# Performance work log

Measured on AMD Instinct MI355X. Metric: run time of the kernel, lower is better.

## Reference

```python
import jax, jax.numpy as jnp
import numpy as np

DIM_U1 = 20
DIM_U2 = 20
DZ = 6
BATCH = 4096


def _mlp(x, Wa, ba, Wb, bb, Wc, bc, Wd, bd):
    h = jax.nn.relu(x @ Wa + ba)
    h = jax.nn.relu(h @ Wb + bb)
    h = jax.nn.relu(h @ Wc + bc)
    return h @ Wd + bd


def setup_inputs() -> dict:
    key = jax.random.key(0)
    ks = jax.random.split(key, 9)

    def lin(k, fan_in, fan_out):
        k1, k2 = jax.random.split(k)
        lim = 1.0 / np.sqrt(fan_in)
        W = jax.random.uniform(k1, (fan_in, fan_out), minval=-lim, maxval=lim, dtype=jnp.float32)
        b = jax.random.uniform(k2, (fan_out,), minval=-lim, maxval=lim, dtype=jnp.float32)
        return W, b

    d = {"x": jax.random.normal(ks[0], (BATCH, DIM_U1), dtype=jnp.float32)}
    dims1 = [(3, 16), (16, 32), (32, 16), (16, 1 + DZ * 3)]
    dims2 = [(3, 16), (16, 32), (32, 16), (16, DZ + 5 * DZ * DZ)]
    names = ["a", "b", "c", "d"]
    for j, (fi, fo) in enumerate(dims1):
        W, b = lin(ks[1 + j], fi, fo)
        d["W1" + names[j]] = W
        d["b1" + names[j]] = b
    for j, (fi, fo) in enumerate(dims2):
        W, b = lin(ks[5 + j], fi, fo)
        d["W2" + names[j]] = W
        d["b2" + names[j]] = b
    return d


def reference(x, W1a, b1a, W1b, b1b, W1c, b1c, W1d, b1d,
              W2a, b2a, W2b, b2b, W2c, b2c, W2d, b2d):
    B = x.shape[0]
    # gather local neighbor triples: [B, dim_u1, 3]
    idx = (jnp.arange(DIM_U1)[:, None] + jnp.arange(-1, 2)[None, :]) % DIM_U1
    xl = x[:, idx]
    out1 = _mlp(xl, W1a, b1a, W1b, b1b, W1c, b1c, W1d, b1d)  # [B, 20, 19]
    out2 = _mlp(xl, W2a, b2a, W2b, b2b, W2c, b2c, W2d, b2d)  # [B, 20, 186]

    f1 = out1[:, :, :1]  # [B, 20, 1]

    # banded scatter for g1: [B, dim_u1, dz*dim_u2]
    rows1 = jnp.arange(DIM_U1)[:, None]
    cols1 = (jnp.arange(3 * DZ)[None, :] + (jnp.arange(DIM_U1)[:, None] - 1) * DZ) % (DZ * DIM_U2)
    g1 = jnp.zeros((B, DIM_U1, DZ * DIM_U2), x.dtype).at[:, rows1, cols1].set(out1[:, :, 1:])

    f2 = out2[:, :, :DZ].reshape(B, DZ * DIM_U2, 1)

    # banded scatter for g2: [B, dz*dim_u2, dz*dim_u2]
    rows2 = jnp.arange(DZ * DIM_U2)[:, None]
    base = (jnp.arange(5 * DZ)[None, :] + (jnp.arange(DIM_U2)[:, None] - 2) * DZ) % (DZ * DIM_U2)  # [20, 30]
    cols2 = jnp.repeat(base, DZ, axis=0)  # [120, 30]
    vals2 = out2[:, :, DZ:].reshape(B, DZ * DIM_U2, 5 * DZ)
    g2 = jnp.zeros((B, DZ * DIM_U2, DZ * DIM_U2), x.dtype).at[:, rows2, cols2].set(vals2)

    return (f1, g1, f2, g2)
```

## Files before the change

kernel.cpp:

```cpp
#include <hip/hip_runtime.h>

typedef unsigned short u16;
typedef unsigned int   u32;

#define U 20

struct Ptrs { const float* p[16]; };

static __device__ __forceinline__ float bf2f(u16 h) {
    u32 u = ((u32)h) << 16;
    float f;
    __builtin_memcpy(&f, &u, 4);
    return f;
}

static __device__ __forceinline__ u16 f2bf(float f) {
    u32 u;
    __builtin_memcpy(&u, &f, 4);
    u32 lsb = (u >> 16) & 1u;
    u += 0x7fffu + lsb;
    return (u16)(u >> 16);
}

static __device__ __forceinline__ float gr(float f) { return bf2f(f2bf(f)); }

__launch_bounds__(256)
__global__ void fused(const float* __restrict__ x, Ptrs pt,
                      float* __restrict__ out, int B, int total) {
    const int tid = threadIdx.x;
    const int t   = blockIdx.x * 256 + tid;

    const size_t g1_off = (size_t)B * 20;
    const size_t f2_off = (size_t)B * 2420;
    const size_t g2_off = (size_t)B * 2540;

    {
        int t0  = blockIdx.x * 256;
        int n_t = total - t0; if (n_t > 256) n_t = 256; if (n_t < 0) n_t = 0;
        float4 z4; z4.x = z4.y = z4.z = z4.w = 0.f;
        float4* z1 = reinterpret_cast<float4*>(out + g1_off + (size_t)t0 * 120);
        int c1 = n_t * 30;
        for (int idx = tid; idx < c1; idx += 256) z1[idx] = z4;
        float4* z2 = reinterpret_cast<float4*>(out + g2_off + (size_t)t0 * 720);
        int c2 = n_t * 180;
        for (int idx = tid; idx < c2; idx += 256) z2[idx] = z4;
    }
    __syncthreads();
    if (t >= total) return;

    const int b = t / U;
    const int i = t - b * U;

    const float* W1a = pt.p[0];  const float* b1a = pt.p[1];
    const float* W1b = pt.p[2];  const float* b1b = pt.p[3];
    const float* W1c = pt.p[4];  const float* b1c = pt.p[5];
    const float* W1d = pt.p[6];  const float* b1d = pt.p[7];
    const float* W2a = pt.p[8];  const float* b2a = pt.p[9];
    const float* W2b = pt.p[10]; const float* b2b = pt.p[11];
    const float* W2c = pt.p[12]; const float* b2c = pt.p[13];
    const float* W2d = pt.p[14]; const float* b2d = pt.p[15];

    float* g1row  = out + g1_off + (size_t)t * 120;
    float* g2rows = out + g2_off + (size_t)t * 720;

    const float* xb = x + (size_t)b * U;
    int im = (i == 0)     ? U - 1 : i - 1;
    int ip = (i == U - 1) ? 0     : i + 1;
    float v0 = xb[im], v1 = xb[i], v2 = xb[ip];

    float h1[16], h2[32], h3[16];

    #pragma unroll
    for (int n = 0; n < 16; n++)
        h1[n] = fmaxf(b1a[n] + v0 * W1a[n] + v1 * W1a[16 + n] + v2 * W1a[32 + n], 0.f);

    #pragma unroll
    for (int n = 0; n < 32; n++) h2[n] = b1b[n];
    #pragma unroll
    for (int k = 0; k < 16; k++) {
        float hk = h1[k];
        #pragma unroll
        for (int n = 0; n < 32; n++) h2[n] += hk * W1b[k * 32 + n];
    }
    #pragma unroll
    for (int n = 0; n < 32; n++) h2[n] = fmaxf(h2[n], 0.f);

    #pragma unroll
    for (int n = 0; n < 16; n++) h3[n] = b1c[n];
    #pragma unroll
    for (int k = 0; k < 32; k++) {
        float hk = h2[k];
        #pragma unroll
        for (int n = 0; n < 16; n++) h3[n] += hk * W1c[k * 16 + n];
    }
    #pragma unroll
    for (int n = 0; n < 16; n++) h3[n] = fmaxf(h3[n], 0.f);

    {
        float o1[19];
        #pragma unroll
        for (int n = 0; n < 19; n++) o1[n] = b1d[n];
        #pragma unroll
        for (int k = 0; k < 16; k++) {
            float hk = h3[k];
            #pragma unroll
            for (int n = 0; n < 19; n++) o1[n] += hk * W1d[k * 19 + n];
        }
        out[t] = gr(o1[0]);
        #pragma unroll
        for (int j = 0; j < 3; j++) {
            int cc = i - 1 + j;
            if (cc < 0)  cc += U;
            if (cc >= U) cc -= U;
            float2* d = reinterpret_cast<float2*>(g1row + cc * 6);
            #pragma unroll
            for (int m = 0; m < 3; m++) {
                float2 v; v.x = gr(o1[1 + j * 6 + 2 * m]);
                          v.y = gr(o1[1 + j * 6 + 2 * m + 1]);
                d[m] = v;
            }
        }
    }

    #pragma unroll
    for (int n = 0; n < 16; n++)
        h1[n] = fmaxf(b2a[n] + v0 * W2a[n] + v1 * W2a[16 + n] + v2 * W2a[32 + n], 0.f);

    #pragma unroll
    for (int n = 0; n < 32; n++) h2[n] = b2b[n];
    #pragma unroll
    for (int k = 0; k < 16; k++) {
        float hk = h1[k];
        #pragma unroll
        for (int n = 0; n < 32; n++) h2[n] += hk * W2b[k * 32 + n];
    }
    #pragma unroll
    for (int n = 0; n < 32; n++) h2[n] = fmaxf(h2[n], 0.f);

    #pragma unroll
    for (int n = 0; n < 16; n++) h3[n] = b2c[n];
    #pragma unroll
    for (int k = 0; k < 32; k++) {
        float hk = h2[k];
        #pragma unroll
        for (int n = 0; n < 16; n++) h3[n] += hk * W2c[k * 16 + n];
    }
    #pragma unroll
    for (int n = 0; n < 16; n++) h3[n] = fmaxf(h3[n], 0.f);

    {
        float o2a[6];
        #pragma unroll
        for (int n = 0; n < 6; n++) o2a[n] = b2d[n];
        #pragma unroll
        for (int k = 0; k < 16; k++) {
            float hk = h3[k];
            #pragma unroll
            for (int n = 0; n < 6; n++) o2a[n] += hk * W2d[k * 186 + n];
        }
        float2* d = reinterpret_cast<float2*>(out + f2_off + (size_t)t * 6);
        #pragma unroll
        for (int m = 0; m < 3; m++) {
            float2 v; v.x = gr(o2a[2 * m]); v.y = gr(o2a[2 * m + 1]);
            d[m] = v;
        }
    }

    for (int z = 0; z < 6; z++) {
        float o2[30];
        #pragma unroll
        for (int n = 0; n < 30; n++) o2[n] = b2d[6 + z * 30 + n];
        #pragma unroll
        for (int k = 0; k < 16; k++) {
            float hk = h3[k];
            #pragma unroll
            for (int n = 0; n < 30; n++) o2[n] += hk * W2d[k * 186 + 6 + z * 30 + n];
        }
        float* row = g2rows + z * 120;
        #pragma unroll
        for (int j = 0; j < 5; j++) {
            int cc = i - 2 + j;
            if (cc < 0)  cc += U;
            if (cc >= U) cc -= U;
            float2* d = reinterpret_cast<float2*>(row + cc * 6);
            #pragma unroll
            for (int m = 0; m < 3; m++) {
                float2 v; v.x = gr(o2[j * 6 + 2 * m]);
                          v.y = gr(o2[j * 6 + 2 * m + 1]);
                d[m] = v;
            }
        }
    }
}

extern "C" void kernel_launch(void* const* d_in, const int* in_sizes, int n_in,
                              void* d_out, int out_size, void* d_ws, size_t ws_size,
                              hipStream_t stream) {
    const float* x = (const float*)d_in[0];
    Ptrs pt;
    for (int a = 0; a < 16; a++) pt.p[a] = (const float*)d_in[1 + a];

    int total = in_sizes[0];
    int B = total / U;

    int blocks = (total + 255) / 256;
    fused<<<blocks, 256, 0, stream>>>(x, pt, (float*)d_out, B, total);
}
```

Measured before the change: 389.4 us.

## Stage outputs in LDS per batch row and split MLP heads across threads

Each block now handles one batch element, assigning 8 threads per position. One thread computes MLP1, one computes the f2 head, and six compute one g2 row block each, instead of one thread doing everything serially. Outputs, including zeros, are assembled in about 68KB of shared memory and written to global memory as coalesced float4 streams. This replaces the earlier global zero-fill followed by scattered float2 stores. The trade-off is that the MLP2 trunk is recomputed 7 times per position, 96 of 256 threads sit idle during compute, and the large LDS footprint limits occupancy.

```diff
diff --git a/kernel.cpp b/kernel.cpp
--- a/kernel.cpp
+++ b/kernel.cpp
@@ -26,169 +26,207 @@
 
 __launch_bounds__(256)
 __global__ void fused(const float* __restrict__ x, Ptrs pt,
-                      float* __restrict__ out, int B, int total) {
+                      float* __restrict__ out, int B) {
+    __shared__ __align__(16) float lds[16940];
     const int tid = threadIdx.x;
-    const int t   = blockIdx.x * 256 + tid;
+    const int b   = blockIdx.x;
+
+    float* s_f1 = lds;
+    float* s_f2 = lds + 20;
+    float* s_g1 = lds + 140;
+    float* s_g2 = lds + 2540;
+
+    const int  i = tid >> 3;
+    const int  s = tid & 7;
+    float v0 = 0.f, v1 = 0.f, v2 = 0.f;
+    if (tid < 160) {
+        const float* xb = x + (size_t)b * U;
+        int im = (i == 0)     ? U - 1 : i - 1;
+        int ip = (i == U - 1) ? 0     : i + 1;
+        v0 = xb[im]; v1 = xb[i]; v2 = xb[ip];
+    }
+
+    {
+        float4 z; z.x = z.y = z.z = z.w = 0.f;
+        float4* zp = reinterpret_cast<float4*>(s_g1);
+        #pragma unroll
+        for (int it = 0; it < 17; ++it) {
+            int idx = it * 256 + tid;
+            if (idx < 4200) zp[idx] = z;
+        }
+    }
+    __syncthreads();
+
+    if (tid < 160) {
+        float h1[16], h2[32], h3[16];
+
+        if (s == 0) {
+            const float* W1a = pt.p[0];  const float* b1a = pt.p[1];
+            const float* W1b = pt.p[2];  const float* b1b = pt.p[3];
+            const float* W1c = pt.p[4];  const float* b1c = pt.p[5];
+            const float* W1d = pt.p[6];  const float* b1d = pt.p[7];
+
+            #pragma unroll
+            for (int n = 0; n < 16; n++)
+                h1[n] = fmaxf(b1a[n] + v0 * W1a[n] + v1 * W1a[16 + n] + v2 * W1a[32 + n], 0.f);
+
+            #pragma unroll
+            for (int n = 0; n < 32; n++) h2[n] = b1b[n];
+            #pragma unroll
+            for (int k = 0; k < 16; k++) {
+                float hk = h1[k];
+                #pragma unroll
+                for (int n = 0; n < 32; n++) h2[n] += hk * W1b[k * 32 + n];
+            }
+            #pragma unroll
+            for (int n = 0; n < 32; n++) h2[n] = fmaxf(h2[n], 0.f);
+
+            #pragma unroll
+            for (int n = 0; n < 16; n++) h3[n] = b1c[n];
+            #pragma unroll
+            for (int k = 0; k < 32; k++) {
+                float hk = h2[k];
+                #pragma unroll
+                for (int n = 0; n < 16; n++) h3[n] += hk * W1c[k * 16 + n];
+            }
+            #pragma unroll
+            for (int n = 0; n < 16; n++) h3[n] = fmaxf(h3[n], 0.f);
+
+            float o1[19];
+            #pragma unroll
+            for (int n = 0; n < 19; n++) o1[n] = b1d[n];
+            #pragma unroll
+            for (int k = 0; k < 16; k++) {
+                float hk = h3[k];
+                #pragma unroll
+                for (int n = 0; n < 19; n++) o1[n] += hk * W1d[k * 19 + n];
+            }
+            s_f1[i] = gr(o1[0]);
+            float* row = s_g1 + i * 120;
+            #pragma unroll
+            for (int j = 0; j < 3; j++) {
+                int cc = i - 1 + j;
+                if (cc < 0)  cc += U;
+                if (cc >= U) cc -= U;
+                float2* d = reinterpret_cast<float2*>(row + cc * 6);
+                #pragma unroll
+                for (int m = 0; m < 3; m++) {
+                    float2 v; v.x = gr(o1[1 + j * 6 + 2 * m]);
+                              v.y = gr(o1[1 + j * 6 + 2 * m + 1]);
+                    d[m] = v;
+                }
+            }
+        } else {
+            const float* W2a = pt.p[8];  const float* b2a = pt.p[9];
+            const float* W2b = pt.p[10]; const float* b2b = pt.p[11];
+            const float* W2c = pt.p[12]; const float* b2c = pt.p[13];
+            const float* W2d = pt.p[14]; const float* b2d = pt.p[15];
+
+            #pragma unroll
+            for (int n = 0; n < 16; n++)
+                h1[n] = fmaxf(b2a[n] + v0 * W2a[n] + v1 * W2a[16 + n] + v2 * W2a[32 + n], 0.f);
+
+            #pragma unroll
+            for (int n = 0; n < 32; n++) h2[n] = b2b[n];
+            #pragma unroll
+            for (int k = 0; k < 16; k++) {
+                float hk = h1[k];
+                #pragma unroll
+                for (int n = 0; n < 32; n++) h2[n] += hk * W2b[k * 32 + n];
+            }
+            #pragma unroll
+            for (int n = 0; n < 32; n++) h2[n] = fmaxf(h2[n], 0.f);
+
+            #pragma unroll
+            for (int n = 0; n < 16; n++) h3[n] = b2c[n];
+            #pragma unroll
+            for (int k = 0; k < 32; k++) {
+                float hk = h2[k];
+                #pragma unroll
+                for (int n = 0; n < 16; n++) h3[n] += hk * W2c[k * 16 + n];
+            }
+            #pragma unroll
+            for (int n = 0; n < 16; n++) h3[n] = fmaxf(h3[n], 0.f);
+
+            if (s == 1) {
+                float o2a[6];
+                #pragma unroll
+                for (int n = 0; n < 6; n++) o2a[n] = b2d[n];
+                #pragma unroll
+                for (int k = 0; k < 16; k++) {
+                    float hk = h3[k];
+                    #pragma unroll
+                    for (int n = 0; n < 6; n++) o2a[n] += hk * W2d[k * 186 + n];
+                }
+                float2* d = reinterpret_cast<float2*>(s_f2 + i * 6);
+                #pragma unroll
+                for (int m = 0; m < 3; m++) {
+                    float2 v; v.x = gr(o2a[2 * m]); v.y = gr(o2a[2 * m + 1]);
+                    d[m] = v;
+                }
+            } else {
+                const int z = s - 2;
+                float o2[30];
+                #pragma unroll
+                for (int n = 0; n < 30; n++) o2[n] = b2d[6 + z * 30 + n];
+                #pragma unroll
+                for (int k = 0; k < 16; k++) {
+                    float hk = h3[k];
+                    #pragma unroll
+                    for (int n = 0; n < 30; n++) o2[n] += hk * W2d[k * 186 + 6 + z * 30 + n];
+                }
+                float* row = s_g2 + (i * 6 + z) * 120;
+                #pragma unroll
+                for (int j = 0; j < 5; j++) {
+                    int cc = i - 2 + j;
+                    if (cc < 0)  cc += U;
+                    if (cc >= U) cc -= U;
+                    float2* d = reinterpret_cast<float2*>(row + cc * 6);
+                    #pragma unroll
+                    for (int m = 0; m < 3; m++) {
+                        float2 v; v.x = gr(o2[j * 6 + 2 * m]);
+                                  v.y = gr(o2[j * 6 + 2 * m + 1]);
+                        d[m] = v;
+                    }
+                }
+            }
+        }
+    }
+    __syncthreads();
 
     const size_t g1_off = (size_t)B * 20;
     const size_t f2_off = (size_t)B * 2420;
     const size_t g2_off = (size_t)B * 2540;
 
     {
-        int t0  = blockIdx.x * 256;
-        int n_t = total - t0; if (n_t > 256) n_t = 256; if (n_t < 0) n_t = 0;
-        float4 z4; z4.x = z4.y = z4.z = z4.w = 0.f;
-        float4* z1 = reinterpret_cast<float4*>(out + g1_off + (size_t)t0 * 120);
-        int c1 = n_t * 30;
-        for (int idx = tid; idx < c1; idx += 256) z1[idx] = z4;
-        float4* z2 = reinterpret_cast<float4*>(out + g2_off + (size_t)t0 * 720);
-        int c2 = n_t * 180;
-        for (int idx = tid; idx < c2; idx += 256) z2[idx] = z4;
-    }
-    __syncthreads();
-    if (t >= total) return;
-
-    const int b = t / U;
-    const int i = t - b * U;
-
-    const float* W1a = pt.p[0];  const float* b1a = pt.p[1];
-    const float* W1b = pt.p[2];  const float* b1b = pt.p[3];
-    const float* W1c = pt.p[4];  const float* b1c = pt.p[5];
-    const float* W1d = pt.p[6];  const float* b1d = pt.p[7];
-    const float* W2a = pt.p[8];  const float* b2a = pt.p[9];
-    const float* W2b = pt.p[10]; const float* b2b = pt.p[11];
-    const float* W2c = pt.p[12]; const float* b2c = pt.p[13];
-    const float* W2d = pt.p[14]; const float* b2d = pt.p[15];
-
-    float* g1row  = out + g1_off + (size_t)t * 120;
-    float* g2rows = out + g2_off + (size_t)t * 720;
-
-    const float* xb = x + (size_t)b * U;
-    int im = (i == 0)     ? U - 1 : i - 1;
-    int ip = (i == U - 1) ? 0     : i + 1;
-    float v0 = xb[im], v1 = xb[i], v2 = xb[ip];
-
-    float h1[16], h2[32], h3[16];
-
-    #pragma unroll
-    for (int n = 0; n < 16; n++)
-        h1[n] = fmaxf(b1a[n] + v0 * W1a[n] + v1 * W1a[16 + n] + v2 * W1a[32 + n], 0.f);
-
-    #pragma unroll
-    for (int n = 0; n < 32; n++) h2[n] = b1b[n];
-    #pragma unroll
-    for (int k = 0; k < 16; k++) {
-        float hk = h1[k];
+        const float4* sp = reinterpret_cast<const float4*>(s_g2);
+        float4* dp = reinterpret_cast<float4*>(out + g2_off + (size_t)b * 14400);
         #pragma unroll
-        for (int n = 0; n < 32; n++) h2[n] += hk * W1b[k * 32 + n];
-    }
-    #pragma unroll
-    for (int n = 0; n < 32; n++) h2[n] = fmaxf(h2[n], 0.f);
-
-    #pragma unroll
-    for (int n = 0; n < 16; n++) h3[n] = b1c[n];
-    #pragma unroll
-    for (int k = 0; k < 32; k++) {
-        float hk = h2[k];
+        for (int it = 0; it < 15; ++it) {
+            int idx = it * 256 + tid;
+            if (idx < 3600) dp[idx] = sp[idx];
+        }
+    }
+    {
+        const float4* sp = reinterpret_cast<const float4*>(s_g1);
+        float4* dp = reinterpret_cast<float4*>(out + g1_off + (size_t)b * 2400);
         #pragma unroll
-        for (int n = 0; n < 16; n++) h3[n] += hk * W1c[k * 16 + n];
-    }
-    #pragma unroll
-    for (int n = 0; n < 16; n++) h3[n] = fmaxf(h3[n], 0.f);
-
-    {
-        float o1[19];
-        #pragma unroll
-        for (int n = 0; n < 19; n++) o1[n] = b1d[n];
-        #pragma unroll
-        for (int k = 0; k < 16; k++) {
-            float hk = h3[k];
-            #pragma unroll
-            for (int n = 0; n < 19; n++) o1[n] += hk * W1d[k * 19 + n];
-        }
-        out[t] = gr(o1[0]);
-        #pragma unroll
-        for (int j = 0; j < 3; j++) {
-            int cc = i - 1 + j;
-            if (cc < 0)  cc += U;
-            if (cc >= U) cc -= U;
-            float2* d = reinterpret_cast<float2*>(g1row + cc * 6);
-            #pragma unroll
-            for (int m = 0; m < 3; m++) {
-                float2 v; v.x = gr(o1[1 + j * 6 + 2 * m]);
-                          v.y = gr(o1[1 + j * 6 + 2 * m + 1]);
-                d[m] = v;
-            }
-        }
-    }
-
-    #pragma unroll
-    for (int n = 0; n < 16; n++)
-        h1[n] = fmaxf(b2a[n] + v0 * W2a[n] + v1 * W2a[16 + n] + v2 * W2a[32 + n], 0.f);
-
-    #pragma unroll
-    for (int n = 0; n < 32; n++) h2[n] = b2b[n];
-    #pragma unroll
-    for (int k = 0; k < 16; k++) {
-        float hk = h1[k];
-        #pragma unroll
-        for (int n = 0; n < 32; n++) h2[n] += hk * W2b[k * 32 + n];
-    }
-    #pragma unroll
-    for (int n = 0; n < 32; n++) h2[n] = fmaxf(h2[n], 0.f);
-
-    #pragma unroll
-    for (int n = 0; n < 16; n++) h3[n] = b2c[n];
-    #pragma unroll
-    for (int k = 0; k < 32; k++) {
-        float hk = h2[k];
-        #pragma unroll
-        for (int n = 0; n < 16; n++) h3[n] += hk * W2c[k * 16 + n];
-    }
-    #pragma unroll
-    for (int n = 0; n < 16; n++) h3[n] = fmaxf(h3[n], 0.f);
-
-    {
-        float o2a[6];
-        #pragma unroll
-        for (int n = 0; n < 6; n++) o2a[n] = b2d[n];
-        #pragma unroll
-        for (int k = 0; k < 16; k++) {
-            float hk = h3[k];
-            #pragma unroll
-            for (int n = 0; n < 6; n++) o2a[n] += hk * W2d[k * 186 + n];
-        }
-        float2* d = reinterpret_cast<float2*>(out + f2_off + (size_t)t * 6);
-        #pragma unroll
-        for (int m = 0; m < 3; m++) {
-            float2 v; v.x = gr(o2a[2 * m]); v.y = gr(o2a[2 * m + 1]);
-            d[m] = v;
-        }
-    }
-
-    for (int z = 0; z < 6; z++) {
-        float o2[30];
-        #pragma unroll
-        for (int n = 0; n < 30; n++) o2[n] = b2d[6 + z * 30 + n];
-        #pragma unroll
-        for (int k = 0; k < 16; k++) {
-            float hk = h3[k];
-            #pragma unroll
-            for (int n = 0; n < 30; n++) o2[n] += hk * W2d[k * 186 + 6 + z * 30 + n];
-        }
-        float* row = g2rows + z * 120;
-        #pragma unroll
-        for (int j = 0; j < 5; j++) {
-            int cc = i - 2 + j;
-            if (cc < 0)  cc += U;
-            if (cc >= U) cc -= U;
-            float2* d = reinterpret_cast<float2*>(row + cc * 6);
-            #pragma unroll
-            for (int m = 0; m < 3; m++) {
-                float2 v; v.x = gr(o2[j * 6 + 2 * m]);
-                          v.y = gr(o2[j * 6 + 2 * m + 1]);
-                d[m] = v;
-            }
+        for (int it = 0; it < 3; ++it) {
+            int idx = it * 256 + tid;
+            if (idx < 600) dp[idx] = sp[idx];
+        }
+    }
+    if (tid < 5) {
+        const float4* sp = reinterpret_cast<const float4*>(s_f1);
+        float4* dp = reinterpret_cast<float4*>(out + (size_t)b * 20);
+        dp[tid] = sp[tid];
+    }
+    {
+        int q = tid - 64;
+        if (q >= 0 && q < 30) {
+            const float4* sp = reinterpret_cast<const float4*>(s_f2);
+            float4* dp = reinterpret_cast<float4*>(out + f2_off + (size_t)b * 120);
+            dp[q] = sp[q];
         }
     }
 }
@@ -203,6 +241,5 @@
     int total = in_sizes[0];
     int B = total / U;
 
-    int blocks = (total + 255) / 256;
-    fused<<<blocks, 256, 0, stream>>>(x, pt, (float*)d_out, B, total);
-}
+    fused<<<B, 256, 0, stream>>>(x, pt, (float*)d_out, B);
+}
```

Result: slower. 623.2 us (+60.1%).

## Stage MLP outputs in LDS and write banded outputs as coalesced float4 rows

Applied to the files above, without the earlier changes.

Each block now handles 64 sites with 4 waves: wave 0 runs MLP1, and waves 1-3 each run MLP2 and compute two of its six output groups. Weights are first copied into LDS, with padded strides for the last layers. Results are packed as bf16 into shared memory, then all threads write full output rows (zeros plus band values) as coalesced float4 stores. This replaces the separate zero-fill pass and the scattered float2 stores. In exchange, MLP2's hidden layers are computed three times, and the block needs more LDS and barriers.

```diff
diff --git a/kernel.cpp b/kernel.cpp
--- a/kernel.cpp
+++ b/kernel.cpp
@@ -22,174 +22,233 @@
     return (u16)(u >> 16);
 }
 
-static __device__ __forceinline__ float gr(float f) { return bf2f(f2bf(f)); }
+static __device__ __forceinline__ u32 pack2(float a, float b) {
+    return (u32)f2bf(a) | ((u32)f2bf(b) << 16);
+}
 
 __launch_bounds__(256)
-__global__ void fused(const float* __restrict__ x, Ptrs pt,
-                      float* __restrict__ out, int B, int total) {
+__global__ void fused2(const float* __restrict__ x, Ptrs pt,
+                       float* __restrict__ out, int B) {
+    __shared__ __align__(16) float wl[5824];
+    __shared__ __align__(16) u16 s1[64 * 20];
+    __shared__ __align__(16) u16 s2[64 * 186];
     const int tid = threadIdx.x;
-    const int t   = blockIdx.x * 256 + tid;
+    const int T   = B * U;
+
+    {
+        const float* srcs[14] = { pt.p[0], pt.p[1], pt.p[2], pt.p[3], pt.p[4],
+                                  pt.p[5], pt.p[7],
+                                  pt.p[8], pt.p[9], pt.p[10], pt.p[11],
+                                  pt.p[12], pt.p[13], pt.p[15] };
+        const int offs[14] = { 0, 48, 64, 576, 608, 1120, 1456,
+                               1488, 1536, 1552, 2064, 2096, 2608, 5632 };
+        const int cnts[14] = { 48, 16, 512, 32, 512, 16, 19,
+                               48, 16, 512, 32, 512, 16, 186 };
+        #pragma unroll
+        for (int a = 0; a < 14; a++) {
+            const float* s = srcs[a];
+            const int off = offs[a], c = cnts[a];
+            for (int idx = tid; idx < c; idx += 256)
+                wl[off + idx] = s[idx];
+        }
+        for (int idx = tid; idx < 304; idx += 256) {
+            int r = idx / 19, cl = idx - r * 19;
+            wl[1136 + r * 20 + cl] = pt.p[6][idx];
+        }
+        for (int idx = tid; idx < 2976; idx += 256) {
+            int r = idx / 186, cl = idx - r * 186;
+            wl[2624 + r * 188 + cl] = pt.p[14][idx];
+        }
+    }
+    __syncthreads();
+
+    const int lane = tid & 63;
+    const int w    = tid >> 6;
+    const int t0   = blockIdx.x * 64;
+    const int t    = t0 + lane;
+
+    if (t < T) {
+        const int b = t / U;
+        const int i = t - b * U;
+        const float* xb = x + (size_t)b * U;
+        float v0 = xb[(i == 0) ? U - 1 : i - 1];
+        float v1 = xb[i];
+        float v2 = xb[(i == U - 1) ? 0 : i + 1];
+
+        if (w == 0) {
+            const float* Wa = &wl[0];    const float* ba = &wl[48];
+            const float* Wb = &wl[64];   const float* bb = &wl[576];
+            const float* Wc = &wl[608];  const float* bc = &wl[1120];
+            const float* Wd = &wl[1136]; const float* bd = &wl[1456];
+            float h1[16], h2[32], h3[16];
+
+            #pragma unroll
+            for (int n = 0; n < 16; n++)
+                h1[n] = fmaxf(ba[n] + v0 * Wa[n] + v1 * Wa[16 + n] + v2 * Wa[32 + n], 0.f);
+
+            #pragma unroll
+            for (int n = 0; n < 32; n++) h2[n] = bb[n];
+            #pragma unroll
+            for (int k = 0; k < 16; k++) {
+                float hk = h1[k];
+                #pragma unroll
+                for (int n = 0; n < 32; n++) h2[n] += hk * Wb[k * 32 + n];
+            }
+            #pragma unroll
+            for (int n = 0; n < 32; n++) h2[n] = fmaxf(h2[n], 0.f);
+
+            #pragma unroll
+            for (int n = 0; n < 16; n++) h3[n] = bc[n];
+            #pragma unroll
+            for (int k = 0; k < 32; k++) {
+                float hk = h2[k];
+                #pragma unroll
+                for (int n = 0; n < 16; n++) h3[n] += hk * Wc[k * 16 + n];
+            }
+            #pragma unroll
+            for (int n = 0; n < 16; n++) h3[n] = fmaxf(h3[n], 0.f);
+
+            float o1[19];
+            #pragma unroll
+            for (int n = 0; n < 19; n++) o1[n] = bd[n];
+            #pragma unroll
+            for (int k = 0; k < 16; k++) {
+                float hk = h3[k];
+                #pragma unroll
+                for (int n = 0; n < 19; n++) o1[n] += hk * Wd[k * 20 + n];
+            }
+            #pragma unroll
+            for (int m = 0; m < 9; m++)
+                *reinterpret_cast<u32*>(&s1[lane * 20 + 2 * m]) =
+                    pack2(o1[2 * m], o1[2 * m + 1]);
+            *reinterpret_cast<u32*>(&s1[lane * 20 + 18]) = pack2(o1[18], 0.f);
+        } else {
+            const float* Wa = &wl[1488]; const float* ba = &wl[1536];
+            const float* Wb = &wl[1552]; const float* bb = &wl[2064];
+            const float* Wc = &wl[2096]; const float* bc = &wl[2608];
+            const float* Wd = &wl[2624]; const float* bd = &wl[5632];
+            float h1[16], h2[32], h3[16];
+
+            #pragma unroll
+            for (int n = 0; n < 16; n++)
+                h1[n] = fmaxf(ba[n] + v0 * Wa[n] + v1 * Wa[16 + n] + v2 * Wa[32 + n], 0.f);
+
+            #pragma unroll
+            for (int n = 0; n < 32; n++) h2[n] = bb[n];
+            #pragma unroll
+            for (int k = 0; k < 16; k++) {
+                float hk = h1[k];
+                #pragma unroll
+                for (int n = 0; n < 32; n++) h2[n] += hk * Wb[k * 32 + n];
+            }
+            #pragma unroll
+            for (int n = 0; n < 32; n++) h2[n] = fmaxf(h2[n], 0.f);
+
+            #pragma unroll
+            for (int n = 0; n < 16; n++) h3[n] = bc[n];
+            #pragma unroll
+            for (int k = 0; k < 32; k++) {
+                float hk = h2[k];
+                #pragma unroll
+                for (int n = 0; n < 16; n++) h3[n] += hk * Wc[k * 16 + n];
+            }
+            #pragma unroll
+            for (int n = 0; n < 16; n++) h3[n] = fmaxf(h3[n], 0.f);
+
+            if (w == 1) {
+                float o2a[6];
+                #pragma unroll
+                for (int n = 0; n < 6; n++) o2a[n] = bd[n];
+                #pragma unroll
+                for (int k = 0; k < 16; k++) {
+                    float hk = h3[k];
+                    #pragma unroll
+                    for (int n = 0; n < 6; n++) o2a[n] += hk * Wd[k * 188 + n];
+                }
+                *reinterpret_cast<u32*>(&s2[lane * 186 + 0]) = pack2(o2a[0], o2a[1]);
+                *reinterpret_cast<u32*>(&s2[lane * 186 + 2]) = pack2(o2a[2], o2a[3]);
+                *reinterpret_cast<u32*>(&s2[lane * 186 + 4]) = pack2(o2a[4], o2a[5]);
+            }
+
+            const int zbase = (w - 1) * 2;
+            #pragma unroll
+            for (int zz = 0; zz < 2; zz++) {
+                const int z = zbase + zz;
+                float o2[30];
+                #pragma unroll
+                for (int n = 0; n < 30; n++) o2[n] = bd[6 + z * 30 + n];
+                #pragma unroll
+                for (int k = 0; k < 16; k++) {
+                    float hk = h3[k];
+                    #pragma unroll
+                    for (int n = 0; n < 30; n++) o2[n] += hk * Wd[k * 188 + 6 + z * 30 + n];
+                }
+                #pragma unroll
+                for (int m = 0; m < 15; m++)
+                    *reinterpret_cast<u32*>(&s2[lane * 186 + 6 + z * 30 + 2 * m]) =
+                        pack2(o2[2 * m], o2[2 * m + 1]);
+            }
+        }
+    }
+    __syncthreads();
+
+    int n_t = T - t0; if (n_t > 64) n_t = 64; if (n_t < 0) n_t = 0;
+    const int i0 = t0 % U;
 
     const size_t g1_off = (size_t)B * 20;
     const size_t f2_off = (size_t)B * 2420;
     const size_t g2_off = (size_t)B * 2540;
 
     {
-        int t0  = blockIdx.x * 256;
-        int n_t = total - t0; if (n_t > 256) n_t = 256; if (n_t < 0) n_t = 0;
-        float4 z4; z4.x = z4.y = z4.z = z4.w = 0.f;
-        float4* z1 = reinterpret_cast<float4*>(out + g1_off + (size_t)t0 * 120);
-        int c1 = n_t * 30;
-        for (int idx = tid; idx < c1; idx += 256) z1[idx] = z4;
-        float4* z2 = reinterpret_cast<float4*>(out + g2_off + (size_t)t0 * 720);
-        int c2 = n_t * 180;
-        for (int idx = tid; idx < c2; idx += 256) z2[idx] = z4;
-    }
-    __syncthreads();
-    if (t >= total) return;
-
-    const int b = t / U;
-    const int i = t - b * U;
-
-    const float* W1a = pt.p[0];  const float* b1a = pt.p[1];
-    const float* W1b = pt.p[2];  const float* b1b = pt.p[3];
-    const float* W1c = pt.p[4];  const float* b1c = pt.p[5];
-    const float* W1d = pt.p[6];  const float* b1d = pt.p[7];
-    const float* W2a = pt.p[8];  const float* b2a = pt.p[9];
-    const float* W2b = pt.p[10]; const float* b2b = pt.p[11];
-    const float* W2c = pt.p[12]; const float* b2c = pt.p[13];
-    const float* W2d = pt.p[14]; const float* b2d = pt.p[15];
-
-    float* g1row  = out + g1_off + (size_t)t * 120;
-    float* g2rows = out + g2_off + (size_t)t * 720;
-
-    const float* xb = x + (size_t)b * U;
-    int im = (i == 0)     ? U - 1 : i - 1;
-    int ip = (i == U - 1) ? 0     : i + 1;
-    float v0 = xb[im], v1 = xb[i], v2 = xb[ip];
-
-    float h1[16], h2[32], h3[16];
-
-    #pragma unroll
-    for (int n = 0; n < 16; n++)
-        h1[n] = fmaxf(b1a[n] + v0 * W1a[n] + v1 * W1a[16 + n] + v2 * W1a[32 + n], 0.f);
-
-    #pragma unroll
-    for (int n = 0; n < 32; n++) h2[n] = b1b[n];
-    #pragma unroll
-    for (int k = 0; k < 16; k++) {
-        float hk = h1[k];
-        #pragma unroll
-        for (int n = 0; n < 32; n++) h2[n] += hk * W1b[k * 32 + n];
-    }
-    #pragma unroll
-    for (int n = 0; n < 32; n++) h2[n] = fmaxf(h2[n], 0.f);
-
-    #pragma unroll
-    for (int n = 0; n < 16; n++) h3[n] = b1c[n];
-    #pragma unroll
-    for (int k = 0; k < 32; k++) {
-        float hk = h2[k];
-        #pragma unroll
-        for (int n = 0; n < 16; n++) h3[n] += hk * W1c[k * 16 + n];
-    }
-    #pragma unroll
-    for (int n = 0; n < 16; n++) h3[n] = fmaxf(h3[n], 0.f);
-
-    {
-        float o1[19];
-        #pragma unroll
-        for (int n = 0; n < 19; n++) o1[n] = b1d[n];
-        #pragma unroll
-        for (int k = 0; k < 16; k++) {
-            float hk = h3[k];
-            #pragma unroll
-            for (int n = 0; n < 19; n++) o1[n] += hk * W1d[k * 19 + n];
-        }
-        out[t] = gr(o1[0]);
-        #pragma unroll
-        for (int j = 0; j < 3; j++) {
-            int cc = i - 1 + j;
-            if (cc < 0)  cc += U;
-            if (cc >= U) cc -= U;
-            float2* d = reinterpret_cast<float2*>(g1row + cc * 6);
-            #pragma unroll
-            for (int m = 0; m < 3; m++) {
-                float2 v; v.x = gr(o1[1 + j * 6 + 2 * m]);
-                          v.y = gr(o1[1 + j * 6 + 2 * m + 1]);
-                d[m] = v;
-            }
-        }
-    }
-
-    #pragma unroll
-    for (int n = 0; n < 16; n++)
-        h1[n] = fmaxf(b2a[n] + v0 * W2a[n] + v1 * W2a[16 + n] + v2 * W2a[32 + n], 0.f);
-
-    #pragma unroll
-    for (int n = 0; n < 32; n++) h2[n] = b2b[n];
-    #pragma unroll
-    for (int k = 0; k < 16; k++) {
-        float hk = h1[k];
-        #pragma unroll
-        for (int n = 0; n < 32; n++) h2[n] += hk * W2b[k * 32 + n];
-    }
-    #pragma unroll
-    for (int n = 0; n < 32; n++) h2[n] = fmaxf(h2[n], 0.f);
-
-    #pragma unroll
-    for (int n = 0; n < 16; n++) h3[n] = b2c[n];
-    #pragma unroll
-    for (int k = 0; k < 32; k++) {
-        float hk = h2[k];
-        #pragma unroll
-        for (int n = 0; n < 16; n++) h3[n] += hk * W2c[k * 16 + n];
-    }
-    #pragma unroll
-    for (int n = 0; n < 16; n++) h3[n] = fmaxf(h3[n], 0.f);
-
-    {
-        float o2a[6];
-        #pragma unroll
-        for (int n = 0; n < 6; n++) o2a[n] = b2d[n];
-        #pragma unroll
-        for (int k = 0; k < 16; k++) {
-            float hk = h3[k];
-            #pragma unroll
-            for (int n = 0; n < 6; n++) o2a[n] += hk * W2d[k * 186 + n];
-        }
-        float2* d = reinterpret_cast<float2*>(out + f2_off + (size_t)t * 6);
-        #pragma unroll
-        for (int m = 0; m < 3; m++) {
-            float2 v; v.x = gr(o2a[2 * m]); v.y = gr(o2a[2 * m + 1]);
-            d[m] = v;
-        }
-    }
-
-    for (int z = 0; z < 6; z++) {
-        float o2[30];
-        #pragma unroll
-        for (int n = 0; n < 30; n++) o2[n] = b2d[6 + z * 30 + n];
-        #pragma unroll
-        for (int k = 0; k < 16; k++) {
-            float hk = h3[k];
-            #pragma unroll
-            for (int n = 0; n < 30; n++) o2[n] += hk * W2d[k * 186 + 6 + z * 30 + n];
-        }
-        float* row = g2rows + z * 120;
-        #pragma unroll
-        for (int j = 0; j < 5; j++) {
-            int cc = i - 2 + j;
-            if (cc < 0)  cc += U;
-            if (cc >= U) cc -= U;
-            float2* d = reinterpret_cast<float2*>(row + cc * 6);
-            #pragma unroll
-            for (int m = 0; m < 3; m++) {
-                float2 v; v.x = gr(o2[j * 6 + 2 * m]);
-                          v.y = gr(o2[j * 6 + 2 * m + 1]);
-                d[m] = v;
-            }
-        }
+        float4* og2 = reinterpret_cast<float4*>(out + g2_off + (size_t)t0 * 720);
+        const int c_g2 = n_t * 180;
+        for (int q = tid; q < c_g2; q += 256) {
+            int tl = q / 180;
+            int rq = q - tl * 180;
+            int z  = rq / 30, c4 = rq - z * 30;
+            int i  = i0 + tl; i -= (i / U) * U;
+            int s0 = ((i + 18) % U) * 6;
+            int d0 = 4 * c4 - s0; if (d0 < 0) d0 += 120;
+            const u16* src = &s2[tl * 186 + 6 + z * 30];
+            float vp[4];
+            #pragma unroll
+            for (int k = 0; k < 4; k++) {
+                int d = d0 + k; if (d >= 120) d -= 120;
+                vp[k] = (d < 30) ? bf2f(src[d]) : 0.f;
+            }
+            float4 v; v.x = vp[0]; v.y = vp[1]; v.z = vp[2]; v.w = vp[3];
+            og2[q] = v;
+        }
+    }
+    {
+        float4* og1 = reinterpret_cast<float4*>(out + g1_off + (size_t)t0 * 120);
+        const int c_g1 = n_t * 30;
+        for (int q = tid; q < c_g1; q += 256) {
+            int tl = q / 30, c4 = q - tl * 30;
+            int i  = i0 + tl; i -= (i / U) * U;
+            int s0 = ((i + 19) % U) * 6;
+            int d0 = 4 * c4 - s0; if (d0 < 0) d0 += 120;
+            const u16* src = &s1[tl * 20 + 1];
+            float vp[4];
+            #pragma unroll
+            for (int k = 0; k < 4; k++) {
+                int d = d0 + k; if (d >= 120) d -= 120;
+                vp[k] = (d < 18) ? bf2f(src[d]) : 0.f;
+            }
+            float4 v; v.x = vp[0]; v.y = vp[1]; v.z = vp[2]; v.w = vp[3];
+            og1[q] = v;
+        }
+    }
+    {
+        float* of2 = out + f2_off + (size_t)t0 * 6;
+        const int c_f2 = n_t * 6;
+        for (int q = tid; q < c_f2; q += 256) {
+            int tl = q / 6, zz = q - tl * 6;
+            of2[q] = bf2f(s2[tl * 186 + zz]);
+        }
+    }
+    if (tid < n_t) {
+        out[t0 + tid] = bf2f(s1[tid * 20]);
     }
 }
 
@@ -203,6 +262,6 @@
     int total = in_sizes[0];
     int B = total / U;
 
-    int blocks = (total + 255) / 256;
-    fused<<<blocks, 256, 0, stream>>>(x, pt, (float*)d_out, B, total);
-}
+    int blocks = (total + 63) / 64;
+    fused2<<<blocks, 256, 0, stream>>>(x, pt, (float*)d_out, B);
+}
```

After: 371.4 us. 1.05x faster.
